# Kernel tuning notes

Hardware: AMD Instinct MI355X
Metric: run time of the kernel (lower is better)

## Reference

```python
import jax, jax.numpy as jnp
import numpy as np

OUT_H, OUT_W = 7, 7
SPATIAL_SCALE = 0.0625
SAMPLING_RATIO = 2  # fixed sampling grid (> 0 branch in the original)


def setup_inputs() -> dict:
    key = jax.random.key(0)
    k1, k2, k3, k4, k5 = jax.random.split(key, 5)
    B, C, H, W = 2, 256, 200, 200
    R = 512
    x = jax.random.normal(k1, (B, C, H, W), dtype=jnp.float32)
    img = W / SPATIAL_SCALE  # 3200 px image coordinates
    b = jax.random.randint(k2, (R,), 0, B).astype(jnp.float32)
    x1 = jax.random.uniform(k3, (R,), minval=0.0, maxval=img * 0.8)
    y1 = jax.random.uniform(k4, (R,), minval=0.0, maxval=img * 0.8)
    wh = jax.random.uniform(k5, (R, 2), minval=32.0, maxval=img * 0.2)
    rois = jnp.stack([b, x1, y1, x1 + wh[:, 0], y1 + wh[:, 1]], axis=1).astype(jnp.float32)
    return {"input": x, "rois": rois}


def _axis_coords(start, bin_size, pooled, sr):
    # start: [R]; returns sample coordinates [R, pooled*sr]
    p = jnp.arange(pooled, dtype=jnp.float32)
    i = jnp.arange(sr, dtype=jnp.float32)
    c = (start[:, None, None]
         + p[None, :, None] * bin_size[:, None, None]
         + (i[None, None, :] + 0.5) * bin_size[:, None, None] / sr)
    return c.reshape(start.shape[0], pooled * sr)


def _interp_axis(c, size):
    # per-axis bilinear pieces; c: [R, G]
    valid = (c >= -1.0) & (c <= size)
    cc = jnp.maximum(c, 0.0)
    lo = jnp.floor(cc)
    at_edge = lo >= size - 1
    lo_i = jnp.minimum(lo, size - 1).astype(jnp.int32)
    hi_i = jnp.minimum(lo_i + 1, size - 1)
    frac = jnp.where(at_edge, 0.0, cc - lo)  # l (weight toward hi)
    return lo_i, hi_i, frac, valid


def reference(input, rois):
    R = rois.shape[0]
    B, C, H, W = input.shape
    b = rois[:, 0].astype(jnp.int32)
    x1 = rois[:, 1] * SPATIAL_SCALE
    y1 = rois[:, 2] * SPATIAL_SCALE
    x2 = rois[:, 3] * SPATIAL_SCALE
    y2 = rois[:, 4] * SPATIAL_SCALE
    roi_w = jnp.maximum(x2 - x1, 1.0)
    roi_h = jnp.maximum(y2 - y1, 1.0)
    bin_w = roi_w / OUT_W
    bin_h = roi_h / OUT_H

    ys = _axis_coords(y1, bin_h, OUT_H, SAMPLING_RATIO)  # [R, Yg]
    xs = _axis_coords(x1, bin_w, OUT_W, SAMPLING_RATIO)  # [R, Xg]
    yl, yh, ly, vy = _interp_axis(ys, H)
    xl, xh, lx, vx = _interp_axis(xs, W)
    hy, hx = 1.0 - ly, 1.0 - lx

    bb = b[:, None, None]
    # advanced indexing -> [R, Yg, Xg, C]
    v1 = input[bb, :, yl[:, :, None], xl[:, None, :]]
    v2 = input[bb, :, yl[:, :, None], xh[:, None, :]]
    v3 = input[bb, :, yh[:, :, None], xl[:, None, :]]
    v4 = input[bb, :, yh[:, :, None], xh[:, None, :]]

    w1 = (hy[:, :, None] * hx[:, None, :])[..., None]
    w2 = (hy[:, :, None] * lx[:, None, :])[..., None]
    w3 = (ly[:, :, None] * hx[:, None, :])[..., None]
    w4 = (ly[:, :, None] * lx[:, None, :])[..., None]

    val = w1 * v1 + w2 * v2 + w3 * v3 + w4 * v4
    val = val * (vy[:, :, None] & vx[:, None, :])[..., None]

    S = SAMPLING_RATIO
    val = val.reshape(R, OUT_H, S, OUT_W, S, C).sum(axis=(2, 4)) / (S * S)
    return jnp.transpose(val, (0, 3, 1, 2))  # [R, C, OUT_H, OUT_W]
```

## Files before the change

### kernel.cpp

```cpp
#include <hip/hip_runtime.h>
#include <hip/hip_fp16.h>


#define B_  2
#define C_  256
#define H_  200
#define W_  200
#define R_  512
#define HW_ (H_ * W_)
#define TOTAL_ (B_ * C_ * HW_)
#define BUF_ 1600
#define G_   8

#define HDR_BYTES_  (R_ * 8 * 4)
#define META_BYTES_ (R_ * 4 * 64 * 16)
#define PERM_BYTES_ (R_ * 4)
#define WS_NEED_    (HDR_BYTES_ + META_BYTES_ + PERM_BYTES_)

typedef __attribute__((address_space(3))) unsigned int lds_u32;
typedef const __attribute__((address_space(1))) unsigned int glb_u32;

__device__ __forceinline__ float sample_coord(float start, float bin, int p, int i) {
    return start + (float)p * bin + ((float)i + 0.5f) * bin * 0.5f;
}
__device__ __forceinline__ int lo_clamped(float v, int size) {
    return (int)fminf(floorf(fmaxf(v, 0.0f)), (float)(size - 1));
}
__device__ __forceinline__ unsigned int pack_h2(float a, float b) {
    unsigned short ua = __half_as_ushort(__float2half(a));
    unsigned short ub = __half_as_ushort(__float2half(b));
    return (unsigned int)ua | ((unsigned int)ub << 16);
}
__device__ __forceinline__ float h2f_lo(unsigned int u) {
    return __half2float(__ushort_as_half((unsigned short)(u & 0xffffu)));
}
__device__ __forceinline__ float h2f_hi(unsigned int u) {
    return __half2float(__ushort_as_half((unsigned short)(u >> 16)));
}

__global__ __launch_bounds__(512) void roialign_sort(
    const float* __restrict__ rois, int* __restrict__ perm) {
    __shared__ unsigned int a[R_];
    int t = threadIdx.x;

    float bf = rois[t * 5 + 0];
    float cx = (rois[t * 5 + 1] + rois[t * 5 + 3]) * 0.5f * 0.0625f;
    float cy = (rois[t * 5 + 2] + rois[t * 5 + 4]) * 0.5f * 0.0625f;
    int bi = (int)bf;
    int ys = min(3, max(0, (int)(cy * (4.0f / 200.0f))));
    int xq = min(255, max(0, (int)(cx * (256.0f / 200.0f))));
    unsigned int key = ((unsigned int)bi << 10) | ((unsigned int)ys << 8) |
                       (unsigned int)xq;
    a[t] = (key << 9) | (unsigned int)t;
    __syncthreads();

    for (int k = 2; k <= R_; k <<= 1) {
        for (int j = k >> 1; j > 0; j >>= 1) {
            int ixj = t ^ j;
            if (ixj > t) {
                bool up = ((t & k) == 0);
                unsigned int av = a[t], bv = a[ixj];
                if ((av > bv) == up) { a[t] = bv; a[ixj] = av; }
            }
            __syncthreads();
        }
    }
    perm[t] = (int)(a[t] & 511u);
}

__global__ __launch_bounds__(64) void roialign_meta(
    const float* __restrict__ rois, int* __restrict__ hdr, int4* __restrict__ meta) {
    int r = blockIdx.x;
    int lane = threadIdx.x;

    const float scale = 0.0625f;
    float bf = rois[r * 5 + 0];
    int   bi = (int)bf;
    float x1 = rois[r * 5 + 1] * scale;
    float y1 = rois[r * 5 + 2] * scale;
    float x2 = rois[r * 5 + 3] * scale;
    float y2 = rois[r * 5 + 4] * scale;
    float bin_w = fmaxf(x2 - x1, 1.0f) * (1.0f / 7.0f);
    float bin_h = fmaxf(y2 - y1, 1.0f) * (1.0f / 7.0f);

    int y0 = lo_clamped(sample_coord(y1, bin_h, 0, 0), H_);
    int yE = min(lo_clamped(sample_coord(y1, bin_h, 6, 1), H_) + 1, H_ - 1);
    int x0 = lo_clamped(sample_coord(x1, bin_w, 0, 0), W_);
    int xE = min(lo_clamped(sample_coord(x1, bin_w, 6, 1), W_) + 1, W_ - 1);
    int rows = yE - y0 + 1;
    int cols = xE - x0 + 1;
    int cols4 = (cols + 3) & ~3;
    if ((cols4 & 31) == 0) cols4 += 4;
    int   T = rows * cols4;
    int   nIter = (T + 255) >> 8;
    float recip = 1.0f / (float)cols4;

    if (lane == 0) {
        int* h = hdr + r * 8;
        h[0] = y0 * W_ + x0;
        h[1] = bi;
        h[2] = cols4;
        h[3] = T;
        h[4] = __float_as_int(recip);
        h[5] = nIter;
        h[6] = 0;
        h[7] = 0;
    }

    int4 o[4] = {{0,0,0,0},{0,0,0,0},{0,0,0,0},{0,0,0,0}};
    if (lane < 49) {
        int ph = lane / 7;
        int pw = lane % 7;

        int   rlo_b[2], rhi_b[2];
        float fy[2];
        bool  vy[2];
#pragma unroll
        for (int iy = 0; iy < 2; ++iy) {
            float y = sample_coord(y1, bin_h, ph, iy);
            vy[iy] = (y >= -1.0f) && (y <= (float)H_);
            float yc = fmaxf(y, 0.0f);
            float yl = floorf(yc);
            bool  edge = yl >= (float)(H_ - 1);
            int   lo = (int)fminf(yl, (float)(H_ - 1));
            int   hi = min(lo + 1, H_ - 1);
            fy[iy] = edge ? 0.0f : (yc - yl);
            rlo_b[iy] = (lo - y0) * cols4 * 4;
            rhi_b[iy] = (hi - y0) * cols4 * 4;
        }
        int   clo_b[2], chi_b[2];
        float fx[2];
        bool  vx[2];
#pragma unroll
        for (int ix = 0; ix < 2; ++ix) {
            float x = sample_coord(x1, bin_w, pw, ix);
            vx[ix] = (x >= -1.0f) && (x <= (float)W_);
            float xc = fmaxf(x, 0.0f);
            float xl = floorf(xc);
            bool  edge = xl >= (float)(W_ - 1);
            int   lo = (int)fminf(xl, (float)(W_ - 1));
            int   hi = min(lo + 1, W_ - 1);
            fx[ix] = edge ? 0.0f : (xc - xl);
            clo_b[ix] = (lo - x0) * 4;
            chi_b[ix] = (hi - x0) * 4;
        }
#pragma unroll
        for (int iy = 0; iy < 2; ++iy)
#pragma unroll
            for (int ix = 0; ix < 2; ++ix) {
                int s = iy * 2 + ix;
                float mk  = (vy[iy] && vx[ix]) ? 0.25f : 0.0f;
                float wy0 = (1.0f - fy[iy]) * mk;
                float wy1 = fy[iy] * mk;
                float wx0 = 1.0f - fx[ix];
                float wx1 = fx[ix];
                o[s].x = rlo_b[iy] | (rhi_b[iy] << 16);
                o[s].y = clo_b[ix] | (chi_b[ix] << 16);
                o[s].z = (int)pack_h2(wy0, wy1);
                o[s].w = (int)pack_h2(wx0, wx1);
            }
    }
#pragma unroll
    for (int s = 0; s < 4; ++s)
        meta[((r * 4 + s) * 64) + lane] = o[s];
}

template<int N> __device__ __forceinline__ void wait_vmcnt() {
    if constexpr (N == 0)      asm volatile("s_waitcnt vmcnt(0)" ::: "memory");
    else if constexpr (N == 1) asm volatile("s_waitcnt vmcnt(1)" ::: "memory");
    else if constexpr (N == 2) asm volatile("s_waitcnt vmcnt(2)" ::: "memory");
    else if constexpr (N == 3) asm volatile("s_waitcnt vmcnt(3)" ::: "memory");
    else if constexpr (N == 4) asm volatile("s_waitcnt vmcnt(4)" ::: "memory");
    else if constexpr (N == 5) asm volatile("s_waitcnt vmcnt(5)" ::: "memory");
    else if constexpr (N == 6) asm volatile("s_waitcnt vmcnt(6)" ::: "memory");
    else                       asm volatile("s_waitcnt vmcnt(7)" ::: "memory");
}

template<int NI>
__device__ __forceinline__ void body(
    const float* __restrict__ input, float* __restrict__ out,
    float* __restrict__ b0, float* __restrict__ b1,
    int lane, int srcbase, int cols4, float recip, int T,
    const int (&off)[16], const float (&wt)[16], int obase) {

    int e4 = lane << 2;

    int so[NI];
#pragma unroll
    for (int i = 0; i < NI; ++i) {
        int e = e4 + (i << 8);
        int row = (int)(((float)e + 0.5f) * recip);
        int col = e - row * cols4;
        so[i] = srcbase + row * W_ + col;
    }

    auto STAGE = [&](float* bp) {
#pragma unroll
        for (int i = 0; i < NI; ++i) {
            if (e4 + (i << 8) < T) {
                int g = min(so[i], TOTAL_ - 4);
                __builtin_amdgcn_global_load_lds((glb_u32*)(input + g),
                                                 (lds_u32*)(bp + (i << 8)), 16, 0, 0);
            }
            so[i] += HW_;
        }
    };

    STAGE(b0);
    STAGE(b1);

    float accs[G_];
#pragma unroll
    for (int k = 0; k < G_; ++k) {
        if (k < G_ - 1) wait_vmcnt<NI>(); else wait_vmcnt<0>();
        float* bp = (k & 1) ? b1 : b0;
        const char* bb = (const char*)bp;
        float a = 0.0f;
#pragma unroll
        for (int s = 0; s < 4; ++s) {
            float v1 = *(const float*)(bb + off[4*s+0]);
            float v2 = *(const float*)(bb + off[4*s+1]);
            float v3 = *(const float*)(bb + off[4*s+2]);
            float v4 = *(const float*)(bb + off[4*s+3]);
            a += wt[4*s+0] * (wt[4*s+2] * v1 + wt[4*s+3] * v2)
               + wt[4*s+1] * (wt[4*s+2] * v3 + wt[4*s+3] * v4);
        }
        accs[k] = a;
        if (k < G_ - 2) {
            asm volatile("s_waitcnt lgkmcnt(0)" ::: "memory");
            __builtin_amdgcn_sched_barrier(0);
            STAGE(bp);
        }
    }

    if (lane < 49) {
#pragma unroll
        for (int k = 0; k < G_; ++k)
            out[obase + k * 49] = accs[k];
    }
}

__global__ __launch_bounds__(64) void roialign_main(
    const float* __restrict__ input, const int* __restrict__ hdr,
    const int4* __restrict__ meta, const int* __restrict__ perm,
    float* __restrict__ out) {
    __shared__ float lds[2][BUF_];
    int lane = threadIdx.x;
    int bidx = blockIdx.x;

    int xcd   = bidx & 7;
    int ixn   = bidx >> 3;
    int rank  = (xcd << 6) | (ixn & 63);
    int cg    = ixn >> 6;
    int r     = perm[rank];
    int c0    = cg << 3;

    int4 m[4];
#pragma unroll
    for (int s = 0; s < 4; ++s)
        m[s] = meta[(((r << 2) + s) << 6) + lane];

    const int* h = hdr + (r << 3);
    int   rel_off = h[0];
    int   bi      = h[1];
    int   cols4   = h[2];
    int   T       = h[3];
    float recip   = __int_as_float(h[4]);
    int   nIter   = __builtin_amdgcn_readfirstlane(h[5]);

    int   off[16];
    float wt[16];
#pragma unroll
    for (int s = 0; s < 4; ++s) {
        unsigned int d0 = (unsigned int)m[s].x;
        unsigned int d1 = (unsigned int)m[s].y;
        int rlo = (int)(d0 & 0xffffu), rhi = (int)(d0 >> 16);
        int clo = (int)(d1 & 0xffffu), chi = (int)(d1 >> 16);
        off[4*s+0] = rlo + clo;
        off[4*s+1] = rlo + chi;
        off[4*s+2] = rhi + clo;
        off[4*s+3] = rhi + chi;
        unsigned int d2 = (unsigned int)m[s].z;
        unsigned int d3 = (unsigned int)m[s].w;
        wt[4*s+0] = h2f_lo(d2);
        wt[4*s+1] = h2f_hi(d2);
        wt[4*s+2] = h2f_lo(d3);
        wt[4*s+3] = h2f_hi(d3);
    }

    int srcbase = (bi * C_ + c0) * HW_ + rel_off;
    int obase   = (r * C_ + c0) * 49 + lane;

    switch (nIter) {
        case 1: body<1>(input, out, lds[0], lds[1], lane, srcbase, cols4, recip, T, off, wt, obase); break;
        case 2: body<2>(input, out, lds[0], lds[1], lane, srcbase, cols4, recip, T, off, wt, obase); break;
        case 3: body<3>(input, out, lds[0], lds[1], lane, srcbase, cols4, recip, T, off, wt, obase); break;
        case 4: body<4>(input, out, lds[0], lds[1], lane, srcbase, cols4, recip, T, off, wt, obase); break;
        case 5: body<5>(input, out, lds[0], lds[1], lane, srcbase, cols4, recip, T, off, wt, obase); break;
        case 6: body<6>(input, out, lds[0], lds[1], lane, srcbase, cols4, recip, T, off, wt, obase); break;
        default: body<7>(input, out, lds[0], lds[1], lane, srcbase, cols4, recip, T, off, wt, obase); break;
    }
}

#define RMAX_   41
#define STRIDE_ 42

__global__ __launch_bounds__(128) void roialign_fallback(
    const float* __restrict__ input,
    const float* __restrict__ rois,
    float* __restrict__ out) {
    __shared__ float lds[2][RMAX_ * STRIDE_];

    int lane = threadIdx.x & 63;
    int wv   = threadIdx.x >> 6;
    int bidx = blockIdx.x;
    int r = bidx >> 7;
    int c = ((bidx & 127) << 1) | wv;

    const float scale = 0.0625f;
    float bf = rois[r * 5 + 0];
    int   bi = (int)bf;
    float x1 = rois[r * 5 + 1] * scale;
    float y1 = rois[r * 5 + 2] * scale;
    float x2 = rois[r * 5 + 3] * scale;
    float y2 = rois[r * 5 + 4] * scale;
    float bin_w = fmaxf(x2 - x1, 1.0f) * (1.0f / 7.0f);
    float bin_h = fmaxf(y2 - y1, 1.0f) * (1.0f / 7.0f);

    int y0 = lo_clamped(sample_coord(y1, bin_h, 0, 0), H_);
    int x0 = lo_clamped(sample_coord(x1, bin_w, 0, 0), W_);
    int yE = min(lo_clamped(sample_coord(y1, bin_h, 6, 1), H_) + 1, H_ - 1);
    int xE = min(lo_clamped(sample_coord(x1, bin_w, 6, 1), W_) + 1, W_ - 1);
    int rows = min(yE - y0 + 1, RMAX_);
    int cols = min(xE - x0 + 1, RMAX_);

    const float* plane = input + ((size_t)bi * C_ + c) * HW_;
    float* myl = lds[wv];
    for (int rr = 0; rr < rows; ++rr) {
        lds_u32* dst = (lds_u32*)(myl + rr * STRIDE_);
        const float* src = plane + (y0 + rr) * W_ + x0 + lane;
        if (lane < cols)
            __builtin_amdgcn_global_load_lds((glb_u32*)src, dst, 4, 0, 0);
    }
    asm volatile("s_waitcnt vmcnt(0)" ::: "memory");
    __builtin_amdgcn_sched_barrier(0);

    if (lane < 49) {
        int ph = lane / 7;
        int pw = lane % 7;
        int   ry[2][2];
        float fy[2];
        bool  vy[2];
#pragma unroll
        for (int iy = 0; iy < 2; ++iy) {
            float y = sample_coord(y1, bin_h, ph, iy);
            vy[iy] = (y >= -1.0f) && (y <= (float)H_);
            float yc = fmaxf(y, 0.0f);
            float yl = floorf(yc);
            bool  edge = yl >= (float)(H_ - 1);
            int   lo = (int)fminf(yl, (float)(H_ - 1));
            int   hi = min(lo + 1, H_ - 1);
            fy[iy] = edge ? 0.0f : (yc - yl);
            ry[iy][0] = (lo - y0) * STRIDE_;
            ry[iy][1] = (hi - y0) * STRIDE_;
        }
        int   rxl[2], rxh[2];
        float fx[2];
        bool  vx[2];
#pragma unroll
        for (int ix = 0; ix < 2; ++ix) {
            float x = sample_coord(x1, bin_w, pw, ix);
            vx[ix] = (x >= -1.0f) && (x <= (float)W_);
            float xc = fmaxf(x, 0.0f);
            float xl = floorf(xc);
            bool  edge = xl >= (float)(W_ - 1);
            int   lo = (int)fminf(xl, (float)(W_ - 1));
            int   hi = min(lo + 1, W_ - 1);
            fx[ix] = edge ? 0.0f : (xc - xl);
            rxl[ix] = lo - x0;
            rxh[ix] = hi - x0;
        }
        float acc = 0.0f;
#pragma unroll
        for (int iy = 0; iy < 2; ++iy) {
            float lyw = fy[iy], hyw = 1.0f - lyw;
#pragma unroll
            for (int ix = 0; ix < 2; ++ix) {
                float lxw = fx[ix], hxw = 1.0f - lxw;
                float msk = (vy[iy] && vx[ix]) ? 1.0f : 0.0f;
                float v1 = myl[ry[iy][0] + rxl[ix]];
                float v2 = myl[ry[iy][0] + rxh[ix]];
                float v3 = myl[ry[iy][1] + rxl[ix]];
                float v4 = myl[ry[iy][1] + rxh[ix]];
                acc += msk * (hyw * hxw * v1 + hyw * lxw * v2 +
                              lyw * hxw * v3 + lyw * lxw * v4);
            }
        }
        out[(r * C_ + c) * 49 + lane] = acc * 0.25f;
    }
}

extern "C" void kernel_launch(void* const* d_in, const int* in_sizes, int n_in,
                              void* d_out, int out_size, void* d_ws, size_t ws_size,
                              hipStream_t stream) {
    const float* input = (const float*)d_in[0];
    const float* rois  = (const float*)d_in[1];
    float* out = (float*)d_out;

    if (ws_size >= (size_t)WS_NEED_) {
        int*  hdr  = (int*)d_ws;
        int4* meta = (int4*)((char*)d_ws + HDR_BYTES_);
        int*  perm = (int*)((char*)d_ws + HDR_BYTES_ + META_BYTES_);
        roialign_sort<<<1, R_, 0, stream>>>(rois, perm);
        roialign_meta<<<R_, 64, 0, stream>>>(rois, hdr, meta);
        roialign_main<<<R_ * 32, 64, 0, stream>>>(input, hdr, meta, perm, out);
    } else {
        roialign_fallback<<<R_ * (C_ / 2), 128, 0, stream>>>(input, rois, out);
    }
}
```

Before: 48.42 us.

## Triple-buffer LDS staging and replace bitonic sort with rank counting

The main kernel now stages three channel buffers ahead instead of two, so more async global-to-LDS loads are in flight while each channel is reduced. The wait counts are adjusted to match. LDS per block rises from 2 to 3 buffers, which could lower occupancy. Separately, the ROI sort kernel drops the barrier-heavy bitonic network and has each thread count how many keys are smaller than its own to find its rank. The keys are unique, so the ranks form a valid permutation.

```diff
diff --git a/kernel.cpp b/kernel.cpp
--- a/kernel.cpp
+++ b/kernel.cpp
@@ -40,7 +40,7 @@
 
 __global__ __launch_bounds__(512) void roialign_sort(
     const float* __restrict__ rois, int* __restrict__ perm) {
-    __shared__ unsigned int a[R_];
+    __shared__ unsigned int keys[R_];
     int t = threadIdx.x;
 
     float bf = rois[t * 5 + 0];
@@ -51,21 +51,15 @@
     int xq = min(255, max(0, (int)(cx * (256.0f / 200.0f))));
     unsigned int key = ((unsigned int)bi << 10) | ((unsigned int)ys << 8) |
                        (unsigned int)xq;
-    a[t] = (key << 9) | (unsigned int)t;
+    unsigned int mykey = (key << 9) | (unsigned int)t;
+    keys[t] = mykey;
     __syncthreads();
 
-    for (int k = 2; k <= R_; k <<= 1) {
-        for (int j = k >> 1; j > 0; j >>= 1) {
-            int ixj = t ^ j;
-            if (ixj > t) {
-                bool up = ((t & k) == 0);
-                unsigned int av = a[t], bv = a[ixj];
-                if ((av > bv) == up) { a[t] = bv; a[ixj] = av; }
-            }
-            __syncthreads();
-        }
-    }
-    perm[t] = (int)(a[t] & 511u);
+    int rank = 0;
+#pragma unroll 8
+    for (int u = 0; u < R_; ++u)
+        rank += (keys[u] < mykey) ? 1 : 0;
+    perm[rank] = t;
 }
 
 __global__ __launch_bounds__(64) void roialign_meta(
@@ -166,20 +160,48 @@
 }
 
 template<int N> __device__ __forceinline__ void wait_vmcnt() {
-    if constexpr (N == 0)      asm volatile("s_waitcnt vmcnt(0)" ::: "memory");
-    else if constexpr (N == 1) asm volatile("s_waitcnt vmcnt(1)" ::: "memory");
-    else if constexpr (N == 2) asm volatile("s_waitcnt vmcnt(2)" ::: "memory");
-    else if constexpr (N == 3) asm volatile("s_waitcnt vmcnt(3)" ::: "memory");
-    else if constexpr (N == 4) asm volatile("s_waitcnt vmcnt(4)" ::: "memory");
-    else if constexpr (N == 5) asm volatile("s_waitcnt vmcnt(5)" ::: "memory");
-    else if constexpr (N == 6) asm volatile("s_waitcnt vmcnt(6)" ::: "memory");
-    else                       asm volatile("s_waitcnt vmcnt(7)" ::: "memory");
+    static_assert(N >= 0 && N <= 14, "vmcnt range");
+    if constexpr (N == 0)       asm volatile("s_waitcnt vmcnt(0)" ::: "memory");
+    else if constexpr (N == 1)  asm volatile("s_waitcnt vmcnt(1)" ::: "memory");
+    else if constexpr (N == 2)  asm volatile("s_waitcnt vmcnt(2)" ::: "memory");
+    else if constexpr (N == 3)  asm volatile("s_waitcnt vmcnt(3)" ::: "memory");
+    else if constexpr (N == 4)  asm volatile("s_waitcnt vmcnt(4)" ::: "memory");
+    else if constexpr (N == 5)  asm volatile("s_waitcnt vmcnt(5)" ::: "memory");
+    else if constexpr (N == 6)  asm volatile("s_waitcnt vmcnt(6)" ::: "memory");
+    else if constexpr (N == 7)  asm volatile("s_waitcnt vmcnt(7)" ::: "memory");
+    else if constexpr (N == 8)  asm volatile("s_waitcnt vmcnt(8)" ::: "memory");
+    else if constexpr (N == 9)  asm volatile("s_waitcnt vmcnt(9)" ::: "memory");
+    else if constexpr (N == 10) asm volatile("s_waitcnt vmcnt(10)" ::: "memory");
+    else if constexpr (N == 11) asm volatile("s_waitcnt vmcnt(11)" ::: "memory");
+    else if constexpr (N == 12) asm volatile("s_waitcnt vmcnt(12)" ::: "memory");
+    else if constexpr (N == 13) asm volatile("s_waitcnt vmcnt(13)" ::: "memory");
+    else                        asm volatile("s_waitcnt vmcnt(14)" ::: "memory");
+}
+__device__ __forceinline__ void drain_lds() {
+    asm volatile("s_waitcnt lgkmcnt(0)" ::: "memory");
+    __builtin_amdgcn_sched_barrier(0);
+}
+
+__device__ __forceinline__ float compute_ch(
+    const float* bp, const int (&off)[16], const float (&wt)[16]) {
+    const char* bb = (const char*)bp;
+    float a = 0.0f;
+#pragma unroll
+    for (int s = 0; s < 4; ++s) {
+        float v1 = *(const float*)(bb + off[4*s+0]);
+        float v2 = *(const float*)(bb + off[4*s+1]);
+        float v3 = *(const float*)(bb + off[4*s+2]);
+        float v4 = *(const float*)(bb + off[4*s+3]);
+        a += wt[4*s+0] * (wt[4*s+2] * v1 + wt[4*s+3] * v2)
+           + wt[4*s+1] * (wt[4*s+2] * v3 + wt[4*s+3] * v4);
+    }
+    return a;
 }
 
 template<int NI>
 __device__ __forceinline__ void body(
     const float* __restrict__ input, float* __restrict__ out,
-    float* __restrict__ b0, float* __restrict__ b1,
+    float* __restrict__ b0, float* __restrict__ b1, float* __restrict__ b2,
     int lane, int srcbase, int cols4, float recip, int T,
     const int (&off)[16], const float (&wt)[16], int obase) {
 
@@ -208,30 +230,17 @@
 
     STAGE(b0);
     STAGE(b1);
+    STAGE(b2);
 
     float accs[G_];
-#pragma unroll
-    for (int k = 0; k < G_; ++k) {
-        if (k < G_ - 1) wait_vmcnt<NI>(); else wait_vmcnt<0>();
-        float* bp = (k & 1) ? b1 : b0;
-        const char* bb = (const char*)bp;
-        float a = 0.0f;
-#pragma unroll
-        for (int s = 0; s < 4; ++s) {
-            float v1 = *(const float*)(bb + off[4*s+0]);
-            float v2 = *(const float*)(bb + off[4*s+1]);
-            float v3 = *(const float*)(bb + off[4*s+2]);
-            float v4 = *(const float*)(bb + off[4*s+3]);
-            a += wt[4*s+0] * (wt[4*s+2] * v1 + wt[4*s+3] * v2)
-               + wt[4*s+1] * (wt[4*s+2] * v3 + wt[4*s+3] * v4);
-        }
-        accs[k] = a;
-        if (k < G_ - 2) {
-            asm volatile("s_waitcnt lgkmcnt(0)" ::: "memory");
-            __builtin_amdgcn_sched_barrier(0);
-            STAGE(bp);
-        }
-    }
+    wait_vmcnt<2*NI>(); accs[0] = compute_ch(b0, off, wt); drain_lds(); STAGE(b0);
+    wait_vmcnt<2*NI>(); accs[1] = compute_ch(b1, off, wt); drain_lds(); STAGE(b1);
+    wait_vmcnt<2*NI>(); accs[2] = compute_ch(b2, off, wt); drain_lds(); STAGE(b2);
+    wait_vmcnt<2*NI>(); accs[3] = compute_ch(b0, off, wt); drain_lds(); STAGE(b0);
+    wait_vmcnt<2*NI>(); accs[4] = compute_ch(b1, off, wt); drain_lds(); STAGE(b1);
+    wait_vmcnt<2*NI>(); accs[5] = compute_ch(b2, off, wt);
+    wait_vmcnt<NI>();   accs[6] = compute_ch(b0, off, wt);
+    wait_vmcnt<0>();    accs[7] = compute_ch(b1, off, wt);
 
     if (lane < 49) {
 #pragma unroll
@@ -244,7 +253,7 @@
     const float* __restrict__ input, const int* __restrict__ hdr,
     const int4* __restrict__ meta, const int* __restrict__ perm,
     float* __restrict__ out) {
-    __shared__ float lds[2][BUF_];
+    __shared__ float lds[3][BUF_];
     int lane = threadIdx.x;
     int bidx = blockIdx.x;
 
@@ -292,13 +301,13 @@
     int obase   = (r * C_ + c0) * 49 + lane;
 
     switch (nIter) {
-        case 1: body<1>(input, out, lds[0], lds[1], lane, srcbase, cols4, recip, T, off, wt, obase); break;
-        case 2: body<2>(input, out, lds[0], lds[1], lane, srcbase, cols4, recip, T, off, wt, obase); break;
-        case 3: body<3>(input, out, lds[0], lds[1], lane, srcbase, cols4, recip, T, off, wt, obase); break;
-        case 4: body<4>(input, out, lds[0], lds[1], lane, srcbase, cols4, recip, T, off, wt, obase); break;
-        case 5: body<5>(input, out, lds[0], lds[1], lane, srcbase, cols4, recip, T, off, wt, obase); break;
-        case 6: body<6>(input, out, lds[0], lds[1], lane, srcbase, cols4, recip, T, off, wt, obase); break;
-        default: body<7>(input, out, lds[0], lds[1], lane, srcbase, cols4, recip, T, off, wt, obase); break;
+        case 1: body<1>(input, out, lds[0], lds[1], lds[2], lane, srcbase, cols4, recip, T, off, wt, obase); break;
+        case 2: body<2>(input, out, lds[0], lds[1], lds[2], lane, srcbase, cols4, recip, T, off, wt, obase); break;
+        case 3: body<3>(input, out, lds[0], lds[1], lds[2], lane, srcbase, cols4, recip, T, off, wt, obase); break;
+        case 4: body<4>(input, out, lds[0], lds[1], lds[2], lane, srcbase, cols4, recip, T, off, wt, obase); break;
+        case 5: body<5>(input, out, lds[0], lds[1], lds[2], lane, srcbase, cols4, recip, T, off, wt, obase); break;
+        case 6: body<6>(input, out, lds[0], lds[1], lds[2], lane, srcbase, cols4, recip, T, off, wt, obase); break;
+        default: body<7>(input, out, lds[0], lds[1], lds[2], lane, srcbase, cols4, recip, T, off, wt, obase); break;
     }
 }
 
```

Measured after the change: 49.82 us. 1.03x slower.

## Replace bitonic sort with rank-by-count and pack two channel groups per block

Applied to the files above, without the earlier changes.

The single-block bitonic sort, with its many barriers, is replaced by a counting rank: each thread compares its key against all 512 keys in shared memory and writes its index at that rank. Keys are unique because the index sits in the low bits, so ranks do not collide. The main kernel now runs 128-thread blocks holding two independent waves, each with its own double-buffered LDS region for an adjacent channel group, which halves the grid size. Both waves share the same ROI's metadata load pattern, but the larger LDS per block could change occupancy.

```diff
diff --git a/kernel.cpp b/kernel.cpp
--- a/kernel.cpp
+++ b/kernel.cpp
@@ -40,7 +40,7 @@
 
 __global__ __launch_bounds__(512) void roialign_sort(
     const float* __restrict__ rois, int* __restrict__ perm) {
-    __shared__ unsigned int a[R_];
+    __shared__ unsigned int keys[R_];
     int t = threadIdx.x;
 
     float bf = rois[t * 5 + 0];
@@ -51,21 +51,15 @@
     int xq = min(255, max(0, (int)(cx * (256.0f / 200.0f))));
     unsigned int key = ((unsigned int)bi << 10) | ((unsigned int)ys << 8) |
                        (unsigned int)xq;
-    a[t] = (key << 9) | (unsigned int)t;
+    unsigned int mykey = (key << 9) | (unsigned int)t;
+    keys[t] = mykey;
     __syncthreads();
 
-    for (int k = 2; k <= R_; k <<= 1) {
-        for (int j = k >> 1; j > 0; j >>= 1) {
-            int ixj = t ^ j;
-            if (ixj > t) {
-                bool up = ((t & k) == 0);
-                unsigned int av = a[t], bv = a[ixj];
-                if ((av > bv) == up) { a[t] = bv; a[ixj] = av; }
-            }
-            __syncthreads();
-        }
-    }
-    perm[t] = (int)(a[t] & 511u);
+    int rank = 0;
+#pragma unroll 8
+    for (int u = 0; u < R_; ++u)
+        rank += (keys[u] < mykey) ? 1 : 0;
+    perm[rank] = t;
 }
 
 __global__ __launch_bounds__(64) void roialign_meta(
@@ -240,20 +234,23 @@
     }
 }
 
-__global__ __launch_bounds__(64) void roialign_main(
+__global__ __launch_bounds__(128) void roialign_main(
     const float* __restrict__ input, const int* __restrict__ hdr,
     const int4* __restrict__ meta, const int* __restrict__ perm,
     float* __restrict__ out) {
-    __shared__ float lds[2][BUF_];
-    int lane = threadIdx.x;
+    __shared__ float lds[2][2][BUF_];
+    int tid  = threadIdx.x;
+    int lane = tid & 63;
+    int w    = tid >> 6;
     int bidx = blockIdx.x;
 
-    int xcd   = bidx & 7;
-    int ixn   = bidx >> 3;
-    int rank  = (xcd << 6) | (ixn & 63);
-    int cg    = ixn >> 6;
-    int r     = perm[rank];
-    int c0    = cg << 3;
+    int xcd    = bidx & 7;
+    int ixn    = bidx >> 3;
+    int rank   = (xcd << 6) | (ixn & 63);
+    int cgpair = ixn >> 6;
+    int r      = perm[rank];
+    int cg     = (cgpair << 1) | w;
+    int c0     = cg << 3;
 
     int4 m[4];
 #pragma unroll
@@ -290,15 +287,17 @@
 
     int srcbase = (bi * C_ + c0) * HW_ + rel_off;
     int obase   = (r * C_ + c0) * 49 + lane;
+    float* b0 = lds[w][0];
+    float* b1 = lds[w][1];
 
     switch (nIter) {
-        case 1: body<1>(input, out, lds[0], lds[1], lane, srcbase, cols4, recip, T, off, wt, obase); break;
-        case 2: body<2>(input, out, lds[0], lds[1], lane, srcbase, cols4, recip, T, off, wt, obase); break;
-        case 3: body<3>(input, out, lds[0], lds[1], lane, srcbase, cols4, recip, T, off, wt, obase); break;
-        case 4: body<4>(input, out, lds[0], lds[1], lane, srcbase, cols4, recip, T, off, wt, obase); break;
-        case 5: body<5>(input, out, lds[0], lds[1], lane, srcbase, cols4, recip, T, off, wt, obase); break;
-        case 6: body<6>(input, out, lds[0], lds[1], lane, srcbase, cols4, recip, T, off, wt, obase); break;
-        default: body<7>(input, out, lds[0], lds[1], lane, srcbase, cols4, recip, T, off, wt, obase); break;
+        case 1: body<1>(input, out, b0, b1, lane, srcbase, cols4, recip, T, off, wt, obase); break;
+        case 2: body<2>(input, out, b0, b1, lane, srcbase, cols4, recip, T, off, wt, obase); break;
+        case 3: body<3>(input, out, b0, b1, lane, srcbase, cols4, recip, T, off, wt, obase); break;
+        case 4: body<4>(input, out, b0, b1, lane, srcbase, cols4, recip, T, off, wt, obase); break;
+        case 5: body<5>(input, out, b0, b1, lane, srcbase, cols4, recip, T, off, wt, obase); break;
+        case 6: body<6>(input, out, b0, b1, lane, srcbase, cols4, recip, T, off, wt, obase); break;
+        default: body<7>(input, out, b0, b1, lane, srcbase, cols4, recip, T, off, wt, obase); break;
     }
 }
 
@@ -413,7 +412,7 @@
         int*  perm = (int*)((char*)d_ws + HDR_BYTES_ + META_BYTES_);
         roialign_sort<<<1, R_, 0, stream>>>(rois, perm);
         roialign_meta<<<R_, 64, 0, stream>>>(rois, hdr, meta);
-        roialign_main<<<R_ * 32, 64, 0, stream>>>(input, hdr, meta, perm, out);
+        roialign_main<<<R_ * 16, 128, 0, stream>>>(input, hdr, meta, perm, out);
     } else {
         roialign_fallback<<<R_ * (C_ / 2), 128, 0, stream>>>(input, rois, out);
     }
```

Measured after the change: 53.34 us. +10.2%, slower.
